# Kernel tuning notes

Hardware: AMD Instinct MI355X
Metric: run time of the kernel (lower is better)

Reference implementation:

```python
import jax, jax.numpy as jnp
import numpy as np

N_NODES = 100000
N_EDGES = 1600000
N_REL = 8
IN_CH = 64
HIDDEN = 64
OUT_CH = 32


def setup_inputs() -> dict:
    key = jax.random.key(0)
    ks = jax.random.split(key, 10)
    s_in = 1.0 / np.sqrt(IN_CH)
    s_h = 1.0 / np.sqrt(HIDDEN)
    return {
        "x": jax.random.normal(ks[0], (N_NODES, IN_CH), dtype=jnp.float32),
        "edge_index": jax.random.randint(ks[1], (2, N_EDGES), 0, N_NODES, dtype=jnp.int64),
        "edge_type": jax.random.randint(ks[2], (N_EDGES,), 0, N_REL, dtype=jnp.int64),
        "W0": jax.random.normal(ks[3], (N_REL, IN_CH, HIDDEN), dtype=jnp.float32) * s_in,
        "Q0": jax.random.normal(ks[4], (HIDDEN, 1), dtype=jnp.float32) * s_h,
        "K0": jax.random.normal(ks[5], (HIDDEN, 1), dtype=jnp.float32) * s_h,
        "b0": jnp.zeros((HIDDEN,), dtype=jnp.float32),
        "W1": jax.random.normal(ks[6], (N_REL, HIDDEN, OUT_CH), dtype=jnp.float32) * s_h,
        "Q1": jax.random.normal(ks[7], (OUT_CH, 1), dtype=jnp.float32) * (1.0 / np.sqrt(OUT_CH)),
        "K1": jax.random.normal(ks[8], (OUT_CH, 1), dtype=jnp.float32) * (1.0 / np.sqrt(OUT_CH)),
        "b1": jnp.zeros((OUT_CH,), dtype=jnp.float32),
    }


def rgat_conv(x, src, dst, et, W, Q, K, b, n_nodes):
    # relation-typed transform of all nodes: [R, N, out]
    xw = jnp.einsum("ni,rio->rno", x, W)
    # per-node, per-relation attention logits (heads=1, dim=1)
    q = jnp.einsum("rno,od->rnd", xw, Q)[..., 0]  # [R, N]
    k = jnp.einsum("rno,od->rnd", xw, K)[..., 0]  # [R, N]
    # additive self-attention, leaky_relu slope 0.2 (PyG RGATConv default)
    alpha = jax.nn.leaky_relu(q[et, dst] + k[et, src], negative_slope=0.2)  # [E]
    # across-relation segment softmax over incoming edges of each dst node
    amax = jax.ops.segment_max(alpha, dst, num_segments=n_nodes)
    a = jnp.exp(alpha - amax[dst])
    denom = jax.ops.segment_sum(a, dst, num_segments=n_nodes)
    a = a / (denom[dst] + 1e-16)
    # weighted scatter-add aggregation of transformed source features
    msg = a[:, None] * xw[et, src]  # [E, out]
    return jax.ops.segment_sum(msg, dst, num_segments=n_nodes) + b


def reference(x, edge_index, edge_type, W0, Q0, K0, b0, W1, Q1, K1, b1):
    src, dst = edge_index[0], edge_index[1]
    n = x.shape[0]
    h = rgat_conv(x, src, dst, edge_type, W0, Q0, K0, b0, n)
    h = jax.nn.relu(h)  # dropout p=0.0 -> identity
    out = rgat_conv(h, src, dst, edge_type, W1, Q1, K1, b1, n)
    return out
```

## Files before the change

### kernel.cpp

```cpp
#include <hip/hip_runtime.h>
#include <hip/hip_bf16.h>
#include <math.h>


#define CSR_CHUNK 2048

__global__ void k_bhist(const int* __restrict__ dst, int* __restrict__ bcount,
                        int E, int NB) {
    __shared__ int h[1024];
    int t = threadIdx.x;
    for (int i = t; i < NB; i += 256) h[i] = 0;
    __syncthreads();
    int e0 = blockIdx.x * CSR_CHUNK;
    int e1 = min(e0 + CSR_CHUNK, E);
    for (int i = e0 + t; i < e1; i += 256) atomicAdd(&h[dst[i] >> 7], 1);
    __syncthreads();
    for (int i = t; i < NB; i += 256) {
        int c = h[i];
        if (c) atomicAdd(&bcount[i], c);
    }
}

__global__ void k_bscan(const int* __restrict__ bcount, int* __restrict__ bstart,
                        int* __restrict__ gcur, int* __restrict__ rowptr,
                        int NB, int N, int E) {
    __shared__ int s[1024];
    int t = threadIdx.x;
    int v = (t < NB) ? bcount[t] : 0;
    s[t] = v;
    __syncthreads();
    for (int off = 1; off < 1024; off <<= 1) {
        int a = (t >= off) ? s[t - off] : 0;
        __syncthreads();
        s[t] += a;
        __syncthreads();
    }
    int excl = s[t] - v;
    if (t < NB) {
        bstart[t] = excl;
        gcur[t] = excl;
    }
    if (t == 0) {
        bstart[NB] = E;
        rowptr[N] = E;
    }
}

__global__ void k_bscatter(const int* __restrict__ src, const int* __restrict__ dst,
                           const int* __restrict__ et, int* __restrict__ gcur,
                           unsigned* __restrict__ ebuf, int E, int NB) {
    __shared__ int h[1024];
    __shared__ int basearr[1024];
    int t = threadIdx.x;
    for (int i = t; i < NB; i += 256) h[i] = 0;
    __syncthreads();
    int e0 = blockIdx.x * CSR_CHUNK;
    int e1 = min(e0 + CSR_CHUNK, E);
    for (int i = e0 + t; i < e1; i += 256) atomicAdd(&h[dst[i] >> 7], 1);
    __syncthreads();
    for (int i = t; i < NB; i += 256) {
        int c = h[i];
        basearr[i] = c ? atomicAdd(&gcur[i], c) : 0;
        h[i] = 0;
    }
    __syncthreads();
    for (int i = e0 + t; i < e1; i += 256) {
        int d = dst[i];
        int b = d >> 7;
        int off = atomicAdd(&h[b], 1);
        ebuf[basearr[b] + off] =
            ((unsigned)(d & 127) << 20) | ((unsigned)et[i] << 17) | (unsigned)src[i];
    }
}

__global__ void k_bsort(const unsigned* __restrict__ ebuf, const int* __restrict__ bstart,
                        int* __restrict__ rowptr, int* __restrict__ csr, int N) {
    __shared__ int lh[256];
    __shared__ int ls[256];
    __shared__ int ss[256];
    int b = blockIdx.x, t = threadIdx.x;
    int e0 = bstart[b], e1 = bstart[b + 1];
    lh[t] = 0;
    __syncthreads();
    for (int i = e0 + t; i < e1; i += 256) atomicAdd(&lh[(ebuf[i] >> 20) & 127], 1);
    __syncthreads();
    int v = lh[t];
    ss[t] = v;
    __syncthreads();
    for (int off = 1; off < 256; off <<= 1) {
        int a = (t >= off) ? ss[t - off] : 0;
        __syncthreads();
        ss[t] += a;
        __syncthreads();
    }
    ls[t] = ss[t] - v;
    int node = b * 128 + t;
    if (t < 128 && node < N) rowptr[node] = e0 + ls[t];
    lh[t] = 0;
    __syncthreads();
    for (int i = e0 + t; i < e1; i += 256) {
        unsigned u = ebuf[i];
        int d = (u >> 20) & 127;
        int off = atomicAdd(&lh[d], 1);
        csr[e0 + ls[d] + off] = (int)(u & 0xFFFFF);
    }
}


__global__ void k_wt2(const float* __restrict__ W, __hip_bfloat16* __restrict__ hi,
                      __hip_bfloat16* __restrict__ lo, int OUT, int total) {
    int t = blockIdx.x * blockDim.x + threadIdx.x;
    if (t < total) {
        int per = 64 * OUT;
        int r = t / per;
        int rem = t % per;
        int i = rem / OUT;
        int o = rem % OUT;
        float v = W[t];
        __hip_bfloat16 h = __float2bfloat16(v);
        __hip_bfloat16 l = __float2bfloat16(v - __bfloat162float(h));
        size_t idx = (size_t)o * 512 + i * 8 + r;
        hi[idx] = h;
        lo[idx] = l;
    }
}

__global__ void k_wqk(const float* W, const float* Qv, const float* Kv,
                      float* wq, float* wk, int OUT) {
    int t = blockIdx.x * blockDim.x + threadIdx.x;
    if (t < 8 * 64) {
        int r = t >> 6, i = t & 63;
        const float* wrow = W + ((size_t)r * 64 + i) * OUT;
        float a = 0.f, b = 0.f;
        for (int o = 0; o < OUT; o++) {
            float w = wrow[o];
            a += w * Qv[o];
            b += w * Kv[o];
        }
        wq[t] = a;
        wk[t] = b;
    }
}

__global__ __launch_bounds__(256) void k_qk2(
        const float* __restrict__ xin, const float* __restrict__ wq,
        const float* __restrict__ wk, float* __restrict__ qn,
        float* __restrict__ kn, unsigned short* __restrict__ xbb, int N) {
    __shared__ float xt[64][65];
    __shared__ float swq[8 * 65], swk[8 * 65];
    int t = threadIdx.x;
    int nb0 = blockIdx.x * 64;
    for (int i = t; i < 512; i += 256) {
        int r = i >> 6, c = i & 63;
        swq[r * 65 + c] = wq[i];
        swk[r * 65 + c] = wk[i];
    }
    for (int i = t; i < 1024; i += 256) {
        int ns = i >> 4;
        int c4 = i & 15;
        int n = nb0 + ns;
        float4 v = {0.f, 0.f, 0.f, 0.f};
        if (n < N) v = ((const float4*)xin)[(size_t)n * 16 + c4];
        xt[ns][c4 * 4 + 0] = v.x;
        xt[ns][c4 * 4 + 1] = v.y;
        xt[ns][c4 * 4 + 2] = v.z;
        xt[ns][c4 * 4 + 3] = v.w;
        if (n < N) {
            __hip_bfloat16 b0 = __float2bfloat16(v.x);
            __hip_bfloat16 b1 = __float2bfloat16(v.y);
            __hip_bfloat16 b2 = __float2bfloat16(v.z);
            __hip_bfloat16 b3 = __float2bfloat16(v.w);
            ushort4 o;
            o.x = *(unsigned short*)&b0;
            o.y = *(unsigned short*)&b1;
            o.z = *(unsigned short*)&b2;
            o.w = *(unsigned short*)&b3;
            *(ushort4*)(xbb + (size_t)n * 64 + c4 * 4) = o;
        }
    }
    __syncthreads();
#pragma unroll
    for (int g = t; g < 512; g += 256) {
        int ns = g >> 3, r = g & 7;
        int n = nb0 + ns;
        if (n < N) {
            float qa = 0.f, ka = 0.f;
#pragma unroll
            for (int i = 0; i < 64; i++) {
                float xv = xt[ns][i];
                qa += xv * swq[r * 65 + i];
                ka += xv * swk[r * 65 + i];
            }
            qn[(size_t)n * 8 + r] = qa;
            kn[(size_t)n * 8 + r] = ka;
        }
    }
}

__global__ void k_agg2(const int* __restrict__ rowptr, const int* __restrict__ csr,
                       const float* __restrict__ qn, const float* __restrict__ kn,
                       const unsigned short* __restrict__ xb,
                       __hip_bfloat16* __restrict__ z, int N) {
    int wid = (blockIdx.x * blockDim.x + threadIdx.x) >> 6;
    int lane = threadIdx.x & 63;
    if (wid >= N) return;
    int r0 = rowptr[wid], r1 = rowptr[wid + 1];

    float qv = (lane < 8) ? qn[wid * 8 + lane] : 0.f;

    float denom = 0.f;
    float a0 = 0.f, a1 = 0.f, a2 = 0.f, a3 = 0.f;
    float a4 = 0.f, a5 = 0.f, a6 = 0.f, a7 = 0.f;

    for (int base = r0; base < r1; base += 64) {
        int s = base + lane;
        int pk = (s < r1) ? csr[s] : 0;
        int src = pk & 0x1FFFF;
        int rel = pk >> 17;
        float q = __shfl(qv, rel, 64);
        float tv = 0.f;
        if (s < r1) {
            float v = q + kn[src * 8 + rel];
            v = (v >= 0.f) ? v : 0.2f * v;
            tv = __expf(v);
        }
        float ts = tv;
#pragma unroll
        for (int off = 32; off > 0; off >>= 1) ts += __shfl_xor(ts, off, 64);
        denom += ts;

        int cnt = min(64, r1 - base);
        int tvi = (int)__float_as_uint(tv);
        for (int j = 0; j < cnt; j += 16) {
            unsigned p[16];
            float t[16];
#pragma unroll
            for (int u = 0; u < 16; u++) {
                p[u] = (unsigned)__builtin_amdgcn_readlane(pk, j + u);
                t[u] = __uint_as_float((unsigned)__builtin_amdgcn_readlane(tvi, j + u));
            }
            unsigned xu[16];
#pragma unroll
            for (int u = 0; u < 16; u++)
                xu[u] = (unsigned)xb[(size_t)(p[u] & 0x1FFFF) * 64 + lane];
#pragma unroll
            for (int u = 0; u < 16; u++) {
                float xv = __uint_as_float(xu[u] << 16);
                float tj = t[u];
                switch (p[u] >> 17) {
                    case 0: a0 += tj * xv; break;
                    case 1: a1 += tj * xv; break;
                    case 2: a2 += tj * xv; break;
                    case 3: a3 += tj * xv; break;
                    case 4: a4 += tj * xv; break;
                    case 5: a5 += tj * xv; break;
                    case 6: a6 += tj * xv; break;
                    case 7: a7 += tj * xv; break;
                }
            }
        }
    }

    float inv = 1.f / (denom + 1e-16f);
    unsigned short u[8];
    float av[8] = {a0, a1, a2, a3, a4, a5, a6, a7};
#pragma unroll
    for (int r = 0; r < 8; r++) {
        __hip_bfloat16 b = __float2bfloat16(av[r] * inv);
        u[r] = *(unsigned short*)&b;
    }
    uint4 pack;
    pack.x = (unsigned)u[0] | ((unsigned)u[1] << 16);
    pack.y = (unsigned)u[2] | ((unsigned)u[3] << 16);
    pack.z = (unsigned)u[4] | ((unsigned)u[5] << 16);
    pack.w = (unsigned)u[6] | ((unsigned)u[7] << 16);
    *(uint4*)((unsigned short*)z + (size_t)wid * 512 + lane * 8) = pack;
}

template <int OUT, bool RELU>
__global__ __launch_bounds__(256) void k_zw(
        const __hip_bfloat16* __restrict__ z,
        const __hip_bfloat16* __restrict__ wthi, const __hip_bfloat16* __restrict__ wtlo,
        const float* __restrict__ bias, float* __restrict__ xout, int N) {
    using v8s = __attribute__((ext_vector_type(8))) short;
    using v4f = __attribute__((ext_vector_type(4))) float;
    constexpr int NT = OUT / 16;
    int wave = threadIdx.x >> 6;
    int lane = threadIdx.x & 63;
    int quad = lane >> 4;
    int l15 = lane & 15;
    int m0 = (blockIdx.x * 4 + wave) * 32;
    if (m0 >= N) return;

    v4f acc[NT][2];
#pragma unroll
    for (int nt = 0; nt < NT; nt++) {
        acc[nt][0] = (v4f){0.f, 0.f, 0.f, 0.f};
        acc[nt][1] = (v4f){0.f, 0.f, 0.f, 0.f};
    }

    const short* zp = (const short*)z;
    const short* wh = (const short*)wthi;
    const short* wl = (const short*)wtlo;
    int n0 = m0 + l15, n1 = m0 + 16 + l15;

    for (int k0 = 0; k0 < 512; k0 += 32) {
        int koff = k0 + quad * 8;
        v8s A0 = {}, A1 = {};
        if (n0 < N) A0 = *(const v8s*)(zp + (size_t)n0 * 512 + koff);
        if (n1 < N) A1 = *(const v8s*)(zp + (size_t)n1 * 512 + koff);
#pragma unroll
        for (int nt = 0; nt < NT; nt++) {
            v8s bh = *(const v8s*)(wh + (size_t)(nt * 16 + l15) * 512 + koff);
            v8s bl = *(const v8s*)(wl + (size_t)(nt * 16 + l15) * 512 + koff);
            acc[nt][0] = __builtin_amdgcn_mfma_f32_16x16x32_bf16(A0, bh, acc[nt][0], 0, 0, 0);
            acc[nt][0] = __builtin_amdgcn_mfma_f32_16x16x32_bf16(A0, bl, acc[nt][0], 0, 0, 0);
            acc[nt][1] = __builtin_amdgcn_mfma_f32_16x16x32_bf16(A1, bh, acc[nt][1], 0, 0, 0);
            acc[nt][1] = __builtin_amdgcn_mfma_f32_16x16x32_bf16(A1, bl, acc[nt][1], 0, 0, 0);
        }
    }

#pragma unroll
    for (int nt = 0; nt < NT; nt++) {
        float bcol = bias[nt * 16 + l15];
#pragma unroll
        for (int mm = 0; mm < 2; mm++) {
#pragma unroll
            for (int g = 0; g < 4; g++) {
                int row = m0 + mm * 16 + quad * 4 + g;
                if (row < N) {
                    float o = acc[nt][mm][g] + bcol;
                    if (RELU) o = fmaxf(o, 0.f);
                    xout[(size_t)row * OUT + nt * 16 + l15] = o;
                }
            }
        }
    }
}


extern "C" void kernel_launch(void* const* d_in, const int* in_sizes, int n_in,
                              void* d_out, int out_size, void* d_ws, size_t ws_size,
                              hipStream_t stream) {
    const float* x   = (const float*)d_in[0];
    const int*   ei  = (const int*)d_in[1];
    const int*   et  = (const int*)d_in[2];
    const float* W0  = (const float*)d_in[3];
    const float* Q0  = (const float*)d_in[4];
    const float* K0  = (const float*)d_in[5];
    const float* b0  = (const float*)d_in[6];
    const float* W1  = (const float*)d_in[7];
    const float* Q1  = (const float*)d_in[8];
    const float* K1  = (const float*)d_in[9];
    const float* b1  = (const float*)d_in[10];
    float* out = (float*)d_out;

    const int N = in_sizes[0] / 64;
    const int E = in_sizes[2];
    const int* src = ei;
    const int* dst = ei + E;
    const int NB = (N + 127) >> 7;

    char* p = (char*)d_ws;
    auto alloc = [&](size_t bytes) -> void* {
        void* r = (void*)p;
        p += ((bytes + 255) / 256) * 256;
        return r;
    };
    int* rowptr   = (int*)alloc((size_t)(N + 1) * 4);
    int* bcount   = (int*)alloc(1025 * 4);
    int* bstart   = (int*)alloc(1025 * 4);
    int* gcur     = (int*)alloc(1025 * 4);
    unsigned* ebuf = (unsigned*)alloc((size_t)E * 4);
    int* csr      = (int*)alloc((size_t)E * 4);
    float* wq     = (float*)alloc(8 * 64 * 4);
    float* wk     = (float*)alloc(8 * 64 * 4);
    float* qn     = (float*)alloc((size_t)N * 8 * 4);
    float* kn     = (float*)alloc((size_t)N * 8 * 4);
    __hip_bfloat16* wthi = (__hip_bfloat16*)alloc((size_t)64 * 512 * 2);
    __hip_bfloat16* wtlo = (__hip_bfloat16*)alloc((size_t)64 * 512 * 2);
    __hip_bfloat16* z    = (__hip_bfloat16*)alloc((size_t)N * 512 * 2);
    float* h      = (float*)alloc((size_t)N * 64 * 4);
    unsigned short* xbb = (unsigned short*)alloc((size_t)N * 64 * 2);

    int nchunks = (E + CSR_CHUNK - 1) / CSR_CHUNK;
    hipMemsetAsync(bcount, 0, (size_t)NB * 4, stream);
    k_bhist<<<nchunks, 256, 0, stream>>>(dst, bcount, E, NB);
    k_bscan<<<1, 1024, 0, stream>>>(bcount, bstart, gcur, rowptr, NB, N, E);
    k_bscatter<<<nchunks, 256, 0, stream>>>(src, dst, et, gcur, ebuf, E, NB);
    k_bsort<<<NB, 256, 0, stream>>>(ebuf, bstart, rowptr, csr, N);

    int naggb = (N * 64 + 255) / 256;
    int nzwb = (N + 127) / 128;
    int nqkb = (N + 63) / 64;

    k_wqk<<<2, 256, 0, stream>>>(W0, Q0, K0, wq, wk, 64);
    k_qk2<<<nqkb, 256, 0, stream>>>(x, wq, wk, qn, kn, xbb, N);
    k_wt2<<<(8 * 64 * 64 + 255) / 256, 256, 0, stream>>>(W0, wthi, wtlo, 64, 8 * 64 * 64);
    k_agg2<<<naggb, 256, 0, stream>>>(rowptr, csr, qn, kn, xbb, z, N);
    k_zw<64, true><<<nzwb, 256, 0, stream>>>(z, wthi, wtlo, b0, h, N);

    k_wqk<<<2, 256, 0, stream>>>(W1, Q1, K1, wq, wk, 32);
    k_qk2<<<nqkb, 256, 0, stream>>>(h, wq, wk, qn, kn, xbb, N);
    k_wt2<<<(8 * 64 * 32 + 255) / 256, 256, 0, stream>>>(W1, wthi, wtlo, 32, 8 * 64 * 32);
    k_agg2<<<naggb, 256, 0, stream>>>(rowptr, csr, qn, kn, xbb, z, N);
    k_zw<32, false><<<nzwb, 256, 0, stream>>>(z, wthi, wtlo, b1, out, N);
}
```

Baseline: 524.1 us.

## Use 256-node CSR buckets and LDS-atomic per-relation accumulation in aggregation

```diff
diff --git a/kernel.cpp b/kernel.cpp
--- a/kernel.cpp
+++ b/kernel.cpp
@@ -3,17 +3,17 @@
 #include <math.h>
 
 
-#define CSR_CHUNK 2048
+#define CSR_CHUNK 8192
 
 __global__ void k_bhist(const int* __restrict__ dst, int* __restrict__ bcount,
                         int E, int NB) {
-    __shared__ int h[1024];
+    __shared__ int h[512];
     int t = threadIdx.x;
     for (int i = t; i < NB; i += 256) h[i] = 0;
     __syncthreads();
     int e0 = blockIdx.x * CSR_CHUNK;
     int e1 = min(e0 + CSR_CHUNK, E);
-    for (int i = e0 + t; i < e1; i += 256) atomicAdd(&h[dst[i] >> 7], 1);
+    for (int i = e0 + t; i < e1; i += 256) atomicAdd(&h[dst[i] >> 8], 1);
     __syncthreads();
     for (int i = t; i < NB; i += 256) {
         int c = h[i];
@@ -24,12 +24,12 @@
 __global__ void k_bscan(const int* __restrict__ bcount, int* __restrict__ bstart,
                         int* __restrict__ gcur, int* __restrict__ rowptr,
                         int NB, int N, int E) {
-    __shared__ int s[1024];
+    __shared__ int s[512];
     int t = threadIdx.x;
     int v = (t < NB) ? bcount[t] : 0;
     s[t] = v;
     __syncthreads();
-    for (int off = 1; off < 1024; off <<= 1) {
+    for (int off = 1; off < 512; off <<= 1) {
         int a = (t >= off) ? s[t - off] : 0;
         __syncthreads();
         s[t] += a;
@@ -49,14 +49,14 @@
 __global__ void k_bscatter(const int* __restrict__ src, const int* __restrict__ dst,
                            const int* __restrict__ et, int* __restrict__ gcur,
                            unsigned* __restrict__ ebuf, int E, int NB) {
-    __shared__ int h[1024];
-    __shared__ int basearr[1024];
+    __shared__ int h[512];
+    __shared__ int basearr[512];
     int t = threadIdx.x;
     for (int i = t; i < NB; i += 256) h[i] = 0;
     __syncthreads();
     int e0 = blockIdx.x * CSR_CHUNK;
     int e1 = min(e0 + CSR_CHUNK, E);
-    for (int i = e0 + t; i < e1; i += 256) atomicAdd(&h[dst[i] >> 7], 1);
+    for (int i = e0 + t; i < e1; i += 256) atomicAdd(&h[dst[i] >> 8], 1);
     __syncthreads();
     for (int i = t; i < NB; i += 256) {
         int c = h[i];
@@ -66,10 +66,10 @@
     __syncthreads();
     for (int i = e0 + t; i < e1; i += 256) {
         int d = dst[i];
-        int b = d >> 7;
+        int b = d >> 8;
         int off = atomicAdd(&h[b], 1);
         ebuf[basearr[b] + off] =
-            ((unsigned)(d & 127) << 20) | ((unsigned)et[i] << 17) | (unsigned)src[i];
+            ((unsigned)(d & 255) << 20) | ((unsigned)et[i] << 17) | (unsigned)src[i];
     }
 }
 
@@ -82,7 +82,7 @@
     int e0 = bstart[b], e1 = bstart[b + 1];
     lh[t] = 0;
     __syncthreads();
-    for (int i = e0 + t; i < e1; i += 256) atomicAdd(&lh[(ebuf[i] >> 20) & 127], 1);
+    for (int i = e0 + t; i < e1; i += 256) atomicAdd(&lh[(ebuf[i] >> 20) & 255], 1);
     __syncthreads();
     int v = lh[t];
     ss[t] = v;
@@ -94,13 +94,13 @@
         __syncthreads();
     }
     ls[t] = ss[t] - v;
-    int node = b * 128 + t;
-    if (t < 128 && node < N) rowptr[node] = e0 + ls[t];
+    int node = b * 256 + t;
+    if (node < N) rowptr[node] = e0 + ls[t];
     lh[t] = 0;
     __syncthreads();
     for (int i = e0 + t; i < e1; i += 256) {
         unsigned u = ebuf[i];
-        int d = (u >> 20) & 127;
+        int d = (u >> 20) & 255;
         int off = atomicAdd(&lh[d], 1);
         csr[e0 + ls[d] + off] = (int)(u & 0xFFFFF);
     }
@@ -197,20 +197,23 @@
     }
 }
 
-__global__ void k_agg2(const int* __restrict__ rowptr, const int* __restrict__ csr,
-                       const float* __restrict__ qn, const float* __restrict__ kn,
-                       const unsigned short* __restrict__ xb,
-                       __hip_bfloat16* __restrict__ z, int N) {
+__global__ __launch_bounds__(256) void k_agg3(
+        const int* __restrict__ rowptr, const int* __restrict__ csr,
+        const float* __restrict__ qn, const float* __restrict__ kn,
+        const unsigned short* __restrict__ xb,
+        __hip_bfloat16* __restrict__ z, int N) {
+    __shared__ float sacc[4 * 8 * 64];
+    int wv = threadIdx.x >> 6;
+    int lane = threadIdx.x & 63;
     int wid = (blockIdx.x * blockDim.x + threadIdx.x) >> 6;
-    int lane = threadIdx.x & 63;
     if (wid >= N) return;
+    float* myacc = &sacc[wv * 512];
+#pragma unroll
+    for (int r = 0; r < 8; r++) myacc[r * 64 + lane] = 0.f;
+
     int r0 = rowptr[wid], r1 = rowptr[wid + 1];
-
     float qv = (lane < 8) ? qn[wid * 8 + lane] : 0.f;
-
     float denom = 0.f;
-    float a0 = 0.f, a1 = 0.f, a2 = 0.f, a3 = 0.f;
-    float a4 = 0.f, a5 = 0.f, a6 = 0.f, a7 = 0.f;
 
     for (int base = r0; base < r1; base += 64) {
         int s = base + lane;
@@ -246,27 +249,16 @@
 #pragma unroll
             for (int u = 0; u < 16; u++) {
                 float xv = __uint_as_float(xu[u] << 16);
-                float tj = t[u];
-                switch (p[u] >> 17) {
-                    case 0: a0 += tj * xv; break;
-                    case 1: a1 += tj * xv; break;
-                    case 2: a2 += tj * xv; break;
-                    case 3: a3 += tj * xv; break;
-                    case 4: a4 += tj * xv; break;
-                    case 5: a5 += tj * xv; break;
-                    case 6: a6 += tj * xv; break;
-                    case 7: a7 += tj * xv; break;
-                }
+                atomicAdd(&myacc[(int)((p[u] >> 17) << 6) + lane], t[u] * xv);
             }
         }
     }
 
     float inv = 1.f / (denom + 1e-16f);
     unsigned short u[8];
-    float av[8] = {a0, a1, a2, a3, a4, a5, a6, a7};
 #pragma unroll
     for (int r = 0; r < 8; r++) {
-        __hip_bfloat16 b = __float2bfloat16(av[r] * inv);
+        __hip_bfloat16 b = __float2bfloat16(myacc[r * 64 + lane] * inv);
         u[r] = *(unsigned short*)&b;
     }
     uint4 pack;
@@ -359,7 +351,7 @@
     const int E = in_sizes[2];
     const int* src = ei;
     const int* dst = ei + E;
-    const int NB = (N + 127) >> 7;
+    const int NB = (N + 255) >> 8;
 
     char* p = (char*)d_ws;
     auto alloc = [&](size_t bytes) -> void* {
@@ -368,9 +360,9 @@
         return r;
     };
     int* rowptr   = (int*)alloc((size_t)(N + 1) * 4);
-    int* bcount   = (int*)alloc(1025 * 4);
-    int* bstart   = (int*)alloc(1025 * 4);
-    int* gcur     = (int*)alloc(1025 * 4);
+    int* bcount   = (int*)alloc(513 * 4);
+    int* bstart   = (int*)alloc(513 * 4);
+    int* gcur     = (int*)alloc(513 * 4);
     unsigned* ebuf = (unsigned*)alloc((size_t)E * 4);
     int* csr      = (int*)alloc((size_t)E * 4);
     float* wq     = (float*)alloc(8 * 64 * 4);
@@ -386,7 +378,7 @@
     int nchunks = (E + CSR_CHUNK - 1) / CSR_CHUNK;
     hipMemsetAsync(bcount, 0, (size_t)NB * 4, stream);
     k_bhist<<<nchunks, 256, 0, stream>>>(dst, bcount, E, NB);
-    k_bscan<<<1, 1024, 0, stream>>>(bcount, bstart, gcur, rowptr, NB, N, E);
+    k_bscan<<<1, 512, 0, stream>>>(bcount, bstart, gcur, rowptr, NB, N, E);
     k_bscatter<<<nchunks, 256, 0, stream>>>(src, dst, et, gcur, ebuf, E, NB);
     k_bsort<<<NB, 256, 0, stream>>>(ebuf, bstart, rowptr, csr, N);
 
@@ -397,12 +389,12 @@
     k_wqk<<<2, 256, 0, stream>>>(W0, Q0, K0, wq, wk, 64);
     k_qk2<<<nqkb, 256, 0, stream>>>(x, wq, wk, qn, kn, xbb, N);
     k_wt2<<<(8 * 64 * 64 + 255) / 256, 256, 0, stream>>>(W0, wthi, wtlo, 64, 8 * 64 * 64);
-    k_agg2<<<naggb, 256, 0, stream>>>(rowptr, csr, qn, kn, xbb, z, N);
+    k_agg3<<<naggb, 256, 0, stream>>>(rowptr, csr, qn, kn, xbb, z, N);
     k_zw<64, true><<<nzwb, 256, 0, stream>>>(z, wthi, wtlo, b0, h, N);
 
     k_wqk<<<2, 256, 0, stream>>>(W1, Q1, K1, wq, wk, 32);
     k_qk2<<<nqkb, 256, 0, stream>>>(h, wq, wk, qn, kn, xbb, N);
     k_wt2<<<(8 * 64 * 32 + 255) / 256, 256, 0, stream>>>(W1, wthi, wtlo, 32, 8 * 64 * 32);
-    k_agg2<<<naggb, 256, 0, stream>>>(rowptr, csr, qn, kn, xbb, z, N);
+    k_agg3<<<naggb, 256, 0, stream>>>(rowptr, csr, qn, kn, xbb, z, N);
     k_zw<32, false><<<nzwb, 256, 0, stream>>>(z, wthi, wtlo, b1, out, N);
 }
```

New measurement: 1.873 ms. 3.57x slower.
